# Optimization experiments

Hardware: AMD Instinct MI355X
Metric: run time of the kernel (lower is better)

The kernel has to match this reference:

```python
import jax, jax.numpy as jnp
import numpy as np

N, E, DIN, ED, H, C = 50000, 800000, 128, 16, 4, 128
HC = H * C
SLOPE = 0.2


def gat_conv(x, ei_src, ei_dst, ea, W, a_src, a_dst, We, a_e, b):
    # x: [N, din]; ea: [E, ed] (self-loops already appended by caller)
    n = x.shape[0]
    h = (x @ W).reshape(n, H, C)                       # [N,H,C]
    al_src = (h * a_src).sum(-1)                       # [N,H]
    al_dst = (h * a_dst).sum(-1)                       # [N,H]
    e = (ea @ We).reshape(-1, H, C)                    # [E,H,C]
    al_e = (e * a_e).sum(-1)                           # [E,H]
    alpha = al_src[ei_src] + al_dst[ei_dst] + al_e     # [E,H]
    alpha = jnp.where(alpha > 0, alpha, SLOPE * alpha)  # LeakyReLU(0.2)
    # per-destination-node segment softmax (stable)
    amax = jax.ops.segment_max(alpha, ei_dst, num_segments=n)
    amax = jnp.where(jnp.isfinite(amax), amax, 0.0)
    ex = jnp.exp(alpha - amax[ei_dst])
    den = jax.ops.segment_sum(ex, ei_dst, num_segments=n)
    alpha = ex / (den[ei_dst] + 1e-16)                 # [E,H]
    msg = h[ei_src] * alpha[:, :, None]                # [E,H,C]
    out = jax.ops.segment_sum(msg, ei_dst, num_segments=n)  # [N,H,C]
    return out.reshape(n, HC) + b


def setup_inputs() -> dict:
    key = jax.random.key(0)
    ks = jax.random.split(key, 16)
    s = 0.05
    inp = {
        "x": jax.random.normal(ks[0], (N, DIN), jnp.float32),
        "edge_index": jax.random.randint(ks[1], (2, E), 0, N, jnp.int64),
        "edge_features": jax.random.normal(ks[2], (E, ED), jnp.float32),
        # layer 1 params
        "W1": jax.random.normal(ks[3], (DIN, HC), jnp.float32) * s,
        "att_src1": jax.random.normal(ks[4], (H, C), jnp.float32) * s,
        "att_dst1": jax.random.normal(ks[5], (H, C), jnp.float32) * s,
        "lin_e1": jax.random.normal(ks[6], (ED, HC), jnp.float32) * s,
        "att_e1": jax.random.normal(ks[7], (H, C), jnp.float32) * s,
        "b1": jnp.zeros((HC,), jnp.float32),
        # layer 2 params
        "W2": jax.random.normal(ks[8], (HC, HC), jnp.float32) * s,
        "att_src2": jax.random.normal(ks[9], (H, C), jnp.float32) * s,
        "att_dst2": jax.random.normal(ks[10], (H, C), jnp.float32) * s,
        "lin_e2": jax.random.normal(ks[11], (ED, HC), jnp.float32) * s,
        "att_e2": jax.random.normal(ks[12], (H, C), jnp.float32) * s,
        "b2": jnp.zeros((HC,), jnp.float32),
    }
    return inp


def reference(x, edge_index, edge_features,
              W1, att_src1, att_dst1, lin_e1, att_e1, b1,
              W2, att_src2, att_dst2, lin_e2, att_e2, b2):
    # add self-loops once (PyG default: add_self_loops=True, edge_attr fill='mean')
    loop = jnp.arange(N, dtype=edge_index.dtype)
    ei_src = jnp.concatenate([edge_index[0], loop])
    ei_dst = jnp.concatenate([edge_index[1], loop])
    mean_ea = edge_features.mean(0)
    ea = jnp.concatenate([edge_features, jnp.broadcast_to(mean_ea, (N, ED))], axis=0)

    h = gat_conv(x, ei_src, ei_dst, ea, W1, att_src1, att_dst1, lin_e1, att_e1, b1)
    h = jax.nn.elu(h)
    h = gat_conv(h, ei_src, ei_dst, ea, W2, att_src2, att_dst2, lin_e2, att_e2, b2)
    return jax.nn.elu(h)
```

## Files before the change

### kernel.cpp

```cpp
#include <hip/hip_runtime.h>
#include <math.h>

#define NNODE 50000
#define NEDGE 800000
#define DINv  128
#define EDv   16
#define NHv   4
#define CHv   128
#define HCv   512
#define SLOPEv 0.2f
#define MEANBLK 512

typedef __attribute__((ext_vector_type(8))) short bf16x8;
typedef __attribute__((ext_vector_type(4))) float f32x4;
typedef __attribute__((address_space(3))) unsigned lds_u32;
typedef const __attribute__((address_space(1))) unsigned glb_u32;

__device__ __forceinline__ ushort f2b(float f) {
  unsigned u = __float_as_uint(f);
  u += 0x7FFF + ((u >> 16) & 1);
  return (ushort)(u >> 16);
}
__device__ __forceinline__ float blo(unsigned u) { return __uint_as_float(u << 16); }
__device__ __forceinline__ float bhi(unsigned u) { return __uint_as_float(u & 0xffff0000u); }

__global__ void detect_kernel(const int* __restrict__ ei, int* __restrict__ flag) {
  __shared__ int bad;
  if (threadIdx.x == 0) bad = 0;
  __syncthreads();
  for (int i = threadIdx.x; i < 2048; i += 256)
    if (ei[2 * i + 1] != 0) bad = 1;
  __syncthreads();
  if (threadIdx.x == 0) flag[0] = bad ? 0 : 1;
}

__device__ __forceinline__ int load_idx(const int* __restrict__ ei, int e, int row, int wide) {
  if (wide) return ei[2 * ((size_t)row * NEDGE + e)];
  return ei[(size_t)row * NEDGE + e];
}

__global__ void count_kernel(const int* __restrict__ ei, const int* __restrict__ flag,
                             int* __restrict__ deg) {
  int e = blockIdx.x * blockDim.x + threadIdx.x;
  if (e < NEDGE) {
    int w = flag[0];
    atomicAdd(&deg[load_idx(ei, e, 1, w)], 1);
  }
}

__global__ __launch_bounds__(1024) void scan_kernel(const int* __restrict__ deg,
                                                    int* __restrict__ row_ptr) {
  __shared__ int wsum[16];
  int tid = threadIdx.x;
  int wid = tid >> 6, lane = tid & 63;
  int carry = 0;
  for (int base = 0; base < NNODE; base += 4096) {
    int idx = base + tid * 4;
    int4 x = make_int4(0, 0, 0, 0);
    if (idx < NNODE) x = *(const int4*)(deg + idx);
    int t0 = x.x, t1 = t0 + x.y, t2 = t1 + x.z, t3 = t2 + x.w;
    int v = t3;
#pragma unroll
    for (int off = 1; off < 64; off <<= 1) {
      int t = __shfl_up(v, off, 64);
      if (lane >= off) v += t;
    }
    if (lane == 63) wsum[wid] = v;
    __syncthreads();
    if (wid == 0) {
      int s = (lane < 16) ? wsum[lane] : 0;
#pragma unroll
      for (int off = 1; off < 16; off <<= 1) {
        int t = __shfl_up(s, off, 64);
        if (lane >= off) s += t;
      }
      if (lane < 16) wsum[lane] = s;
    }
    __syncthreads();
    int woff = wid ? wsum[wid - 1] : 0;
    int excl = carry + woff + v - t3;
    if (idx < NNODE) {
      int4 o = make_int4(excl, excl + t0, excl + t1, excl + t2);
      *(int4*)(row_ptr + idx) = o;
    }
    carry += wsum[15];
    __syncthreads();
  }
  if (tid == 0) row_ptr[NNODE] = carry;
}

__global__ void scatter_kernel(const int* __restrict__ ei, const int* __restrict__ flag,
                               const int* __restrict__ row_ptr, int* __restrict__ cursor,
                               int* __restrict__ src_sorted, int* __restrict__ eid_sorted) {
  int e = blockIdx.x * blockDim.x + threadIdx.x;
  if (e < NEDGE) {
    int w = flag[0];
    int d = load_idx(ei, e, 1, w);
    int s = load_idx(ei, e, 0, w);
    int p = row_ptr[d] + atomicAdd(&cursor[d], 1);
    src_sorted[p] = s;
    eid_sorted[p] = e;
  }
}

__global__ void mean_part_kernel(const float* __restrict__ ea, float* __restrict__ partials) {
  float acc[EDv];
#pragma unroll
  for (int d = 0; d < EDv; d++) acc[d] = 0.f;
  int stride = gridDim.x * blockDim.x;
  for (int r = blockIdx.x * blockDim.x + threadIdx.x; r < NEDGE; r += stride) {
    const float4* p = (const float4*)(ea + (size_t)r * EDv);
#pragma unroll
    for (int q = 0; q < 4; q++) {
      float4 v = p[q];
      acc[q * 4 + 0] += v.x; acc[q * 4 + 1] += v.y;
      acc[q * 4 + 2] += v.z; acc[q * 4 + 3] += v.w;
    }
  }
  __shared__ float red[4][EDv];
  int wid = threadIdx.x >> 6, lane = threadIdx.x & 63;
#pragma unroll
  for (int d = 0; d < EDv; d++) {
    float v = acc[d];
    for (int off = 32; off; off >>= 1) v += __shfl_down(v, off, 64);
    if (lane == 0) red[wid][d] = v;
  }
  __syncthreads();
  if (threadIdx.x < EDv) {
    float v = red[0][threadIdx.x] + red[1][threadIdx.x] + red[2][threadIdx.x] + red[3][threadIdx.x];
    partials[blockIdx.x * EDv + threadIdx.x] = v;
  }
}

__global__ void mean_fold_kernel(const float* __restrict__ partials, float* __restrict__ mean_sum) {
  int tid = threadIdx.x;
  int d = tid & 15, r0 = tid >> 4;
  float v = 0.f;
  for (int r = r0; r < MEANBLK; r += 16) v += partials[r * EDv + d];
  __shared__ float buf[256];
  buf[tid] = v;
  __syncthreads();
  if (r0 < 8) buf[tid] += buf[tid + 128];
  __syncthreads();
  if (r0 < 4) buf[tid] += buf[tid + 64];
  __syncthreads();
  if (r0 < 2) buf[tid] += buf[tid + 32];
  __syncthreads();
  if (r0 == 0) mean_sum[d] = buf[tid] + buf[tid + 16];
}

__global__ void vloop_kernel(const float* __restrict__ We, const float* __restrict__ a_e,
                             const float* __restrict__ mean_sum,
                             float* __restrict__ v, float* __restrict__ loop_al_e) {
  int t = threadIdx.x;
  int d = t >> 2, h = t & 3;
  float s = 0.f;
  for (int c = 0; c < CHv; c++) s += We[(size_t)d * HCv + h * CHv + c] * a_e[h * CHv + c];
  v[d * 4 + h] = s;
  __syncthreads();
  if (t < NHv) {
    float acc = 0.f;
    for (int d2 = 0; d2 < EDv; d2++) acc += (mean_sum[d2] * (1.0f / NEDGE)) * v[d2 * 4 + t];
    loop_al_e[t] = acc;
  }
}

__global__ void ale_kernel(const float* __restrict__ ea, const float* __restrict__ v,
                           float* __restrict__ al_e) {
  __shared__ float sv[EDv * NHv];
  if (threadIdx.x < EDv * NHv) sv[threadIdx.x] = v[threadIdx.x];
  __syncthreads();
  int e = blockIdx.x * blockDim.x + threadIdx.x;
  if (e >= NEDGE) return;
  const float4* p = (const float4*)(ea + (size_t)e * EDv);
  float row[16];
  *(float4*)&row[0] = p[0]; *(float4*)&row[4] = p[1];
  *(float4*)&row[8] = p[2]; *(float4*)&row[12] = p[3];
  float o0 = 0, o1 = 0, o2 = 0, o3 = 0;
#pragma unroll
  for (int d = 0; d < 16; d++) {
    o0 += row[d] * sv[d * 4 + 0];
    o1 += row[d] * sv[d * 4 + 1];
    o2 += row[d] * sv[d * 4 + 2];
    o3 += row[d] * sv[d * 4 + 3];
  }
  ((float4*)al_e)[e] = make_float4(o0, o1, o2, o3);
}

__global__ void apre_kernel(const int* __restrict__ src_sorted, const int* __restrict__ eid_sorted,
                            const float* __restrict__ al_src, const float* __restrict__ al_e,
                            float* __restrict__ ap) {
  int p = blockIdx.x * 256 + threadIdx.x;
  if (p >= NEDGE) return;
  int s = src_sorted[p];
  int e = eid_sorted[p];
  float4 a = ((const float4*)al_src)[s];
  float4 b = ((const float4*)al_e)[e];
  ((float4*)ap)[p] = make_float4(a.x + b.x, a.y + b.y, a.z + b.z, a.w + b.w);
}

__global__ void conv_bf16_kernel(const float* __restrict__ in, ushort* __restrict__ out, int n4) {
  int i = blockIdx.x * 256 + threadIdx.x;
  if (i >= n4) return;
  float4 v = ((const float4*)in)[i];
  ushort4 o;
  o.x = f2b(v.x); o.y = f2b(v.y); o.z = f2b(v.z); o.w = f2b(v.w);
  ((ushort4*)out)[i] = o;
}

__global__ void wt_kernel(const float* __restrict__ W, ushort* __restrict__ Bt, int K) {
  int idx = blockIdx.x * 256 + threadIdx.x;
  if (idx >= K * HCv) return;
  int k = idx >> 9, n = idx & (HCv - 1);
  Bt[(size_t)n * K + k] = f2b(W[idx]);
}

__global__ __launch_bounds__(256) void gemm_mfma_kernel(const ushort* __restrict__ A,
                                                        const ushort* __restrict__ Bt,
                                                        ushort* __restrict__ C, int M, int K,
                                                        const float* __restrict__ a_src,
                                                        const float* __restrict__ a_dst,
                                                        float* __restrict__ al_src,
                                                        float* __restrict__ al_dst) {
  __shared__ ushort As[4][128][8];
  __shared__ ushort Bs[4][128][8];
  __shared__ float ssa[128], ssd[128];
  __shared__ float rsum[2][128][2];
  int tid = threadIdx.x;
  int wid = tid >> 6, lane = tid & 63;

  int nblk = gridDim.x * gridDim.y;
  int j = blockIdx.y * gridDim.x + blockIdx.x;
  int q = nblk >> 3, rem = nblk & 7;
  int xcd = j & 7, idx = j >> 3;
  int d = (xcd < rem) ? xcd * (q + 1) + idx : rem * (q + 1) + (xcd - rem) * q + idx;
  int rb = (d >> 2) * 128, cb = (d & 3) * 128;
  int hblk = cb >> 7;

  int wm = (wid >> 1) * 64, wn = (wid & 1) * 64;
  int lr = lane & 15, lq = lane >> 4;

  if (tid < 128) { ssa[tid] = a_src[cb + tid]; ssd[tid] = a_dst[cb + tid]; }

  f32x4 acc[4][4];
#pragma unroll
  for (int i = 0; i < 4; i++)
#pragma unroll
    for (int jx = 0; jx < 4; jx++) acc[i][jx] = (f32x4){0.f, 0.f, 0.f, 0.f};

  ushort* AsF = &As[0][0][0];
  ushort* BsF = &Bs[0][0][0];

  for (int k0 = 0; k0 < K; k0 += 32) {
#pragma unroll
    for (int s = 0; s < 2; s++) {
      int c = s * 256 + tid;
      int kq = c >> 7, m = c & 127;
      int row = rb + m; if (row >= M) row = M - 1;
      const ushort* gA = A + (size_t)row * K + k0 + kq * 8;
      __builtin_amdgcn_global_load_lds((glb_u32*)gA, (lds_u32*)(AsF + (size_t)c * 8), 16, 0, 0);
    }
#pragma unroll
    for (int s = 0; s < 2; s++) {
      int c = s * 256 + tid;
      int kq = c >> 7, n = c & 127;
      const ushort* gB = Bt + (size_t)(cb + n) * K + k0 + kq * 8;
      __builtin_amdgcn_global_load_lds((glb_u32*)gB, (lds_u32*)(BsF + (size_t)c * 8), 16, 0, 0);
    }
    __syncthreads();
    bf16x8 af[4], bfr[4];
#pragma unroll
    for (int i = 0; i < 4; i++) {
      af[i]  = *(const bf16x8*)&As[lq][wm + i * 16 + lr][0];
      bfr[i] = *(const bf16x8*)&Bs[lq][wn + i * 16 + lr][0];
    }
#pragma unroll
    for (int i = 0; i < 4; i++)
#pragma unroll
      for (int jx = 0; jx < 4; jx++)
        acc[i][jx] = __builtin_amdgcn_mfma_f32_16x16x32_bf16(af[i], bfr[jx], acc[i][jx], 0, 0, 0);
    __syncthreads();
  }

#pragma unroll
  for (int i = 0; i < 4; i++) {
    int rbase = rb + wm + i * 16 + lq * 4;
#pragma unroll
    for (int jx = 0; jx < 4; jx++) {
      int col = cb + wn + jx * 16 + lr;
#pragma unroll
      for (int r = 0; r < 4; r++) {
        int row = rbase + r;
        if (row < M) C[(size_t)row * HCv + col] = f2b(acc[i][jx][r]);
      }
    }
  }

  float sa[4], sd[4];
#pragma unroll
  for (int jx = 0; jx < 4; jx++) {
    int c = wn + jx * 16 + lr;
    sa[jx] = ssa[c]; sd[jx] = ssd[c];
  }
#pragma unroll
  for (int i = 0; i < 4; i++) {
#pragma unroll
    for (int r = 0; r < 4; r++) {
      float s1 = 0.f, s2 = 0.f;
#pragma unroll
      for (int jx = 0; jx < 4; jx++) {
        s1 = fmaf(acc[i][jx][r], sa[jx], s1);
        s2 = fmaf(acc[i][jx][r], sd[jx], s2);
      }
#pragma unroll
      for (int off = 1; off < 16; off <<= 1) {
        s1 += __shfl_xor(s1, off, 16);
        s2 += __shfl_xor(s2, off, 16);
      }
      if (lr == 0) {
        int row = wm + i * 16 + lq * 4 + r;
        rsum[0][row][wn >> 6] = s1;
        rsum[1][row][wn >> 6] = s2;
      }
    }
  }
  __syncthreads();
  if (tid < 128) {
    int row = rb + tid;
    if (row < M) {
      al_src[(size_t)row * 4 + hblk] = rsum[0][tid][0] + rsum[0][tid][1];
      al_dst[(size_t)row * 4 + hblk] = rsum[1][tid][0] + rsum[1][tid][1];
    }
  }
}

__device__ __forceinline__ void fma8(float* acc, float w, uint4 u) {
  acc[0] = fmaf(w, blo(u.x), acc[0]);
  acc[1] = fmaf(w, bhi(u.x), acc[1]);
  acc[2] = fmaf(w, blo(u.y), acc[2]);
  acc[3] = fmaf(w, bhi(u.y), acc[3]);
  acc[4] = fmaf(w, blo(u.z), acc[4]);
  acc[5] = fmaf(w, bhi(u.z), acc[5]);
  acc[6] = fmaf(w, blo(u.w), acc[6]);
  acc[7] = fmaf(w, bhi(u.w), acc[7]);
}

__global__ __launch_bounds__(256) void node_kernel(
    const ushort* __restrict__ hb, const float* __restrict__ al_src,
    const float* __restrict__ al_dst, const float* __restrict__ ap,
    const float* __restrict__ loop_al_e, const int* __restrict__ row_ptr,
    const int* __restrict__ src_sorted, const float* __restrict__ bias,
    float* __restrict__ outf, ushort* __restrict__ outb) {
  int wid = threadIdx.x >> 6, lane = threadIdx.x & 63;
  int n = blockIdx.x * 4 + wid;
  if (n >= NNODE) return;
  int base = row_ptr[n];
  int deg = row_ptr[n + 1] - base;
  int h = lane >> 4;
  int jj = lane & 15;

  float aldh = al_dst[(size_t)n * 4 + h];
  float a0 = al_src[(size_t)n * 4 + h] + aldh + loop_al_e[h];
  float alph = a0 > 0.f ? a0 : SLOPEv * a0;
  float wl = __expf(alph);

  uint4 uself = *((const uint4*)(hb + ((size_t)n << 9)) + lane);

  float acc[8];
#pragma unroll
  for (int q = 0; q < 8; q++) acc[q] = 0.f;
  float den = 0.f;

  for (int cs = 0; cs < deg; cs += 16) {
    int cl = min(16, deg - cs);
    float w = 0.f;
    int sv = 0;
    if (jj < cl) {
      int p = base + cs + jj;
      sv = src_sorted[p];
      float a = ap[(size_t)p * 4 + h] + aldh;
      a = a > 0.f ? a : SLOPEv * a;
      w = __expf(a);
      den += w;
    }
    int cl4 = (cl + 3) & ~3;
    for (int j0 = 0; j0 < cl4; j0 += 4) {
      int s0 = __shfl(sv, j0 + 0, 16);
      int s1 = __shfl(sv, j0 + 1, 16);
      int s2 = __shfl(sv, j0 + 2, 16);
      int s3 = __shfl(sv, j0 + 3, 16);
      float w0 = __shfl(w, j0 + 0, 16);
      float w1 = __shfl(w, j0 + 1, 16);
      float w2 = __shfl(w, j0 + 2, 16);
      float w3 = __shfl(w, j0 + 3, 16);
      uint4 u0 = *((const uint4*)(hb + ((size_t)s0 << 9)) + lane);
      uint4 u1 = *((const uint4*)(hb + ((size_t)s1 << 9)) + lane);
      uint4 u2 = *((const uint4*)(hb + ((size_t)s2 << 9)) + lane);
      uint4 u3 = *((const uint4*)(hb + ((size_t)s3 << 9)) + lane);
      fma8(acc, w0, u0);
      fma8(acc, w1, u1);
      fma8(acc, w2, u2);
      fma8(acc, w3, u3);
    }
  }

  fma8(acc, wl, uself);

#pragma unroll
  for (int off = 8; off; off >>= 1) den += __shfl_xor(den, off, 16);
  den += wl;
  float rden = 1.f / (den + 1e-16f);

  const float4* bp = (const float4*)(bias + lane * 8);
  float4 b0 = bp[0], b1 = bp[1];
  float bv[8] = {b0.x, b0.y, b0.z, b0.w, b1.x, b1.y, b1.z, b1.w};
  float r[8];
#pragma unroll
  for (int q = 0; q < 8; q++) {
    float t = acc[q] * rden + bv[q];
    r[q] = t > 0.f ? t : expm1f(t);
  }
  if (outf) {
    float4* op = (float4*)(outf + (size_t)n * HCv + lane * 8);
    op[0] = make_float4(r[0], r[1], r[2], r[3]);
    op[1] = make_float4(r[4], r[5], r[6], r[7]);
  }
  if (outb) {
    uint4 o;
    o.x = (unsigned)f2b(r[0]) | ((unsigned)f2b(r[1]) << 16);
    o.y = (unsigned)f2b(r[2]) | ((unsigned)f2b(r[3]) << 16);
    o.z = (unsigned)f2b(r[4]) | ((unsigned)f2b(r[5]) << 16);
    o.w = (unsigned)f2b(r[6]) | ((unsigned)f2b(r[7]) << 16);
    ((uint4*)(outb + (size_t)n * HCv))[lane] = o;
  }
}

static inline char* take(char*& p, size_t bytes) {
  char* r = p;
  p += (bytes + 255) & ~(size_t)255;
  return r;
}

extern "C" void kernel_launch(void* const* d_in, const int* in_sizes, int n_in,
                              void* d_out, int out_size, void* d_ws, size_t ws_size,
                              hipStream_t stream) {
  (void)in_sizes; (void)n_in; (void)out_size; (void)ws_size;
  const float* x   = (const float*)d_in[0];
  const int*   ei  = (const int*)d_in[1];
  const float* ea  = (const float*)d_in[2];
  const float* W1  = (const float*)d_in[3];
  const float* as1 = (const float*)d_in[4];
  const float* ad1 = (const float*)d_in[5];
  const float* We1 = (const float*)d_in[6];
  const float* ae1 = (const float*)d_in[7];
  const float* b1  = (const float*)d_in[8];
  const float* W2  = (const float*)d_in[9];
  const float* as2 = (const float*)d_in[10];
  const float* ad2 = (const float*)d_in[11];
  const float* We2 = (const float*)d_in[12];
  const float* ae2 = (const float*)d_in[13];
  const float* b2  = (const float*)d_in[14];
  float* out = (float*)d_out;

  char* p = (char*)d_ws;
  ushort* hb        = (ushort*)take(p, (size_t)NNODE * HCv * 2);
  float* al_src     = (float*)take(p, (size_t)NNODE * 4 * 4);
  float* al_dst     = (float*)take(p, (size_t)NNODE * 4 * 4);
  float* al_e       = (float*)take(p, (size_t)NEDGE * 4 * 4);
  float* ap         = (float*)take(p, (size_t)NEDGE * 4 * 4);
  int*   src_sorted = (int*)take(p, (size_t)NEDGE * 4);
  int*   eid_sorted = (int*)take(p, (size_t)NEDGE * 4);
  int*   row_ptr    = (int*)take(p, (size_t)(NNODE + 1) * 4);
  float* partials   = (float*)take(p, (size_t)MEANBLK * EDv * 4);
  ushort* Bt1       = (ushort*)take(p, (size_t)HCv * DINv * 2);
  ushort* Bt2       = (ushort*)take(p, (size_t)HCv * HCv * 2);
  char* zero_begin = p;
  int*   deg        = (int*)take(p, (size_t)NNODE * 4);
  int*   cursor     = (int*)take(p, (size_t)NNODE * 4);
  size_t zero_len = (size_t)(p - zero_begin);
  float* mean_sum   = (float*)take(p, 16 * 4);
  float* v          = (float*)take(p, 64 * 4);
  float* loop_ale   = (float*)take(p, 4 * 4);
  int*   flag       = (int*)take(p, 4);

  ushort* xb  = (ushort*)d_out;
  ushort* h1b = (ushort*)((char*)d_out + (size_t)16 * 1024 * 1024);

  hipMemsetAsync(zero_begin, 0, zero_len, stream);

  detect_kernel<<<1, 256, 0, stream>>>(ei, flag);
  count_kernel<<<(NEDGE + 255) / 256, 256, 0, stream>>>(ei, flag, deg);
  scan_kernel<<<1, 1024, 0, stream>>>(deg, row_ptr);
  scatter_kernel<<<(NEDGE + 255) / 256, 256, 0, stream>>>(ei, flag, row_ptr, cursor,
                                                          src_sorted, eid_sorted);
  mean_part_kernel<<<MEANBLK, 256, 0, stream>>>(ea, partials);
  mean_fold_kernel<<<1, 256, 0, stream>>>(partials, mean_sum);

  conv_bf16_kernel<<<(NNODE * DINv / 4 + 255) / 256, 256, 0, stream>>>(x, xb, NNODE * DINv / 4);
  wt_kernel<<<(DINv * HCv + 255) / 256, 256, 0, stream>>>(W1, Bt1, DINv);
  wt_kernel<<<(HCv * HCv + 255) / 256, 256, 0, stream>>>(W2, Bt2, HCv);

  vloop_kernel<<<1, 64, 0, stream>>>(We1, ae1, mean_sum, v, loop_ale);
  ale_kernel<<<(NEDGE + 255) / 256, 256, 0, stream>>>(ea, v, al_e);
  gemm_mfma_kernel<<<dim3(HCv / 128, (NNODE + 127) / 128), 256, 0, stream>>>(
      xb, Bt1, hb, NNODE, DINv, as1, ad1, al_src, al_dst);
  apre_kernel<<<(NEDGE + 255) / 256, 256, 0, stream>>>(src_sorted, eid_sorted, al_src, al_e, ap);
  node_kernel<<<(NNODE + 3) / 4, 256, 0, stream>>>(hb, al_src, al_dst, ap, loop_ale, row_ptr,
                                                   src_sorted, b1, (float*)nullptr, h1b);

  vloop_kernel<<<1, 64, 0, stream>>>(We2, ae2, mean_sum, v, loop_ale);
  ale_kernel<<<(NEDGE + 255) / 256, 256, 0, stream>>>(ea, v, al_e);
  gemm_mfma_kernel<<<dim3(HCv / 128, (NNODE + 127) / 128), 256, 0, stream>>>(
      h1b, Bt2, hb, NNODE, HCv, as2, ad2, al_src, al_dst);
  apre_kernel<<<(NEDGE + 255) / 256, 256, 0, stream>>>(src_sorted, eid_sorted, al_src, al_e, ap);
  node_kernel<<<(NNODE + 3) / 4, 256, 0, stream>>>(hb, al_src, al_dst, ap, loop_ale, row_ptr,
                                                   src_sorted, b2, out, (ushort*)nullptr);
}
```

Before: 734.8 us.

## Fuse edge-attention precompute for both layers, drop apre pass, widen GEMM K-step

Scatter now records each edge's sorted position instead of the edge id. A single kernel reads edge features once, computes both layers' edge attention terms directly in sorted order, and accumulates the mean for self-loops. The separate apre pass is removed and node_kernel gathers al_src per edge on the fly. Input/weight conversions and small prep kernels are merged to cut launches, and the GEMM K-step doubles to 64 with larger LDS tiles. The trade-offs are a scattered write in the fused edge kernel, an extra random gather in node_kernel, and more LDS per GEMM block.

```diff
diff --git a/kernel.cpp b/kernel.cpp
--- a/kernel.cpp
+++ b/kernel.cpp
@@ -10,6 +10,7 @@
 #define HCv   512
 #define SLOPEv 0.2f
 #define MEANBLK 512
+#define CONVN (NNODE * DINv / 4)
 
 typedef __attribute__((ext_vector_type(8))) short bf16x8;
 typedef __attribute__((ext_vector_type(4))) float f32x4;
@@ -91,7 +92,7 @@
 
 __global__ void scatter_kernel(const int* __restrict__ ei, const int* __restrict__ flag,
                                const int* __restrict__ row_ptr, int* __restrict__ cursor,
-                               int* __restrict__ src_sorted, int* __restrict__ eid_sorted) {
+                               int* __restrict__ src_sorted, int* __restrict__ pos) {
   int e = blockIdx.x * blockDim.x + threadIdx.x;
   if (e < NEDGE) {
     int w = flag[0];
@@ -99,23 +100,57 @@
     int s = load_idx(ei, e, 0, w);
     int p = row_ptr[d] + atomicAdd(&cursor[d], 1);
     src_sorted[p] = s;
-    eid_sorted[p] = e;
-  }
-}
-
-__global__ void mean_part_kernel(const float* __restrict__ ea, float* __restrict__ partials) {
+    pos[e] = p;
+  }
+}
+
+__global__ void prep_kernel(const float* __restrict__ We1, const float* __restrict__ ae1,
+                            const float* __restrict__ We2, const float* __restrict__ ae2,
+                            float* __restrict__ v1, float* __restrict__ v2) {
+  int t = threadIdx.x;
+  int layer = t >> 6, u = t & 63;
+  int d = u >> 2, h = u & 3;
+  const float* We = layer ? We2 : We1;
+  const float* ae = layer ? ae2 : ae1;
+  float s = 0.f;
+  for (int c = 0; c < CHv; c++) s += We[(size_t)d * HCv + h * CHv + c] * ae[h * CHv + c];
+  (layer ? v2 : v1)[d * 4 + h] = s;
+}
+
+__global__ void ale_both_kernel(const float* __restrict__ ea, const int* __restrict__ pos,
+                                const float* __restrict__ v1, const float* __restrict__ v2,
+                                float* __restrict__ al1, float* __restrict__ al2,
+                                float* __restrict__ partials) {
+  __shared__ float sv1[64], sv2[64];
+  if (threadIdx.x < 64) sv1[threadIdx.x] = v1[threadIdx.x];
+  else if (threadIdx.x < 128) sv2[threadIdx.x - 64] = v2[threadIdx.x - 64];
+  __syncthreads();
   float acc[EDv];
 #pragma unroll
   for (int d = 0; d < EDv; d++) acc[d] = 0.f;
   int stride = gridDim.x * blockDim.x;
-  for (int r = blockIdx.x * blockDim.x + threadIdx.x; r < NEDGE; r += stride) {
-    const float4* p = (const float4*)(ea + (size_t)r * EDv);
-#pragma unroll
-    for (int q = 0; q < 4; q++) {
-      float4 v = p[q];
-      acc[q * 4 + 0] += v.x; acc[q * 4 + 1] += v.y;
-      acc[q * 4 + 2] += v.z; acc[q * 4 + 3] += v.w;
-    }
+  for (int e = blockIdx.x * blockDim.x + threadIdx.x; e < NEDGE; e += stride) {
+    const float4* pr = (const float4*)(ea + (size_t)e * EDv);
+    float row[16];
+    *(float4*)&row[0] = pr[0]; *(float4*)&row[4] = pr[1];
+    *(float4*)&row[8] = pr[2]; *(float4*)&row[12] = pr[3];
+    float a0 = 0, a1 = 0, a2 = 0, a3 = 0;
+    float b0 = 0, b1 = 0, b2 = 0, b3 = 0;
+#pragma unroll
+    for (int d = 0; d < 16; d++) {
+      acc[d] += row[d];
+      a0 += row[d] * sv1[d * 4 + 0];
+      a1 += row[d] * sv1[d * 4 + 1];
+      a2 += row[d] * sv1[d * 4 + 2];
+      a3 += row[d] * sv1[d * 4 + 3];
+      b0 += row[d] * sv2[d * 4 + 0];
+      b1 += row[d] * sv2[d * 4 + 1];
+      b2 += row[d] * sv2[d * 4 + 2];
+      b3 += row[d] * sv2[d * 4 + 3];
+    }
+    int p = pos[e];
+    ((float4*)al1)[p] = make_float4(a0, a1, a2, a3);
+    ((float4*)al2)[p] = make_float4(b0, b1, b2, b3);
   }
   __shared__ float red[4][EDv];
   int wid = threadIdx.x >> 6, lane = threadIdx.x & 63;
@@ -132,12 +167,15 @@
   }
 }
 
-__global__ void mean_fold_kernel(const float* __restrict__ partials, float* __restrict__ mean_sum) {
+__global__ void fold_kernel(const float* __restrict__ partials,
+                            const float* __restrict__ v1, const float* __restrict__ v2,
+                            float* __restrict__ loop1, float* __restrict__ loop2) {
   int tid = threadIdx.x;
   int d = tid & 15, r0 = tid >> 4;
   float v = 0.f;
   for (int r = r0; r < MEANBLK; r += 16) v += partials[r * EDv + d];
   __shared__ float buf[256];
+  __shared__ float ms[16];
   buf[tid] = v;
   __syncthreads();
   if (r0 < 8) buf[tid] += buf[tid + 128];
@@ -146,73 +184,35 @@
   __syncthreads();
   if (r0 < 2) buf[tid] += buf[tid + 32];
   __syncthreads();
-  if (r0 == 0) mean_sum[d] = buf[tid] + buf[tid + 16];
-}
-
-__global__ void vloop_kernel(const float* __restrict__ We, const float* __restrict__ a_e,
-                             const float* __restrict__ mean_sum,
-                             float* __restrict__ v, float* __restrict__ loop_al_e) {
-  int t = threadIdx.x;
-  int d = t >> 2, h = t & 3;
-  float s = 0.f;
-  for (int c = 0; c < CHv; c++) s += We[(size_t)d * HCv + h * CHv + c] * a_e[h * CHv + c];
-  v[d * 4 + h] = s;
-  __syncthreads();
-  if (t < NHv) {
-    float acc = 0.f;
-    for (int d2 = 0; d2 < EDv; d2++) acc += (mean_sum[d2] * (1.0f / NEDGE)) * v[d2 * 4 + t];
-    loop_al_e[t] = acc;
-  }
-}
-
-__global__ void ale_kernel(const float* __restrict__ ea, const float* __restrict__ v,
-                           float* __restrict__ al_e) {
-  __shared__ float sv[EDv * NHv];
-  if (threadIdx.x < EDv * NHv) sv[threadIdx.x] = v[threadIdx.x];
-  __syncthreads();
-  int e = blockIdx.x * blockDim.x + threadIdx.x;
-  if (e >= NEDGE) return;
-  const float4* p = (const float4*)(ea + (size_t)e * EDv);
-  float row[16];
-  *(float4*)&row[0] = p[0]; *(float4*)&row[4] = p[1];
-  *(float4*)&row[8] = p[2]; *(float4*)&row[12] = p[3];
-  float o0 = 0, o1 = 0, o2 = 0, o3 = 0;
-#pragma unroll
-  for (int d = 0; d < 16; d++) {
-    o0 += row[d] * sv[d * 4 + 0];
-    o1 += row[d] * sv[d * 4 + 1];
-    o2 += row[d] * sv[d * 4 + 2];
-    o3 += row[d] * sv[d * 4 + 3];
-  }
-  ((float4*)al_e)[e] = make_float4(o0, o1, o2, o3);
-}
-
-__global__ void apre_kernel(const int* __restrict__ src_sorted, const int* __restrict__ eid_sorted,
-                            const float* __restrict__ al_src, const float* __restrict__ al_e,
-                            float* __restrict__ ap) {
-  int p = blockIdx.x * 256 + threadIdx.x;
-  if (p >= NEDGE) return;
-  int s = src_sorted[p];
-  int e = eid_sorted[p];
-  float4 a = ((const float4*)al_src)[s];
-  float4 b = ((const float4*)al_e)[e];
-  ((float4*)ap)[p] = make_float4(a.x + b.x, a.y + b.y, a.z + b.z, a.w + b.w);
-}
-
-__global__ void conv_bf16_kernel(const float* __restrict__ in, ushort* __restrict__ out, int n4) {
+  if (r0 == 0) ms[d] = (buf[tid] + buf[tid + 16]) * (1.0f / NEDGE);
+  __syncthreads();
+  if (tid < 8) {
+    const float* vv = (tid >> 2) ? v2 : v1;
+    int h = tid & 3;
+    float a = 0.f;
+    for (int d2 = 0; d2 < EDv; d2++) a += ms[d2] * vv[d2 * 4 + h];
+    ((tid >> 2) ? loop2 : loop1)[h] = a;
+  }
+}
+
+__global__ void convwt_kernel(const float* __restrict__ x, const float* __restrict__ W1,
+                              const float* __restrict__ W2, ushort* __restrict__ xb,
+                              ushort* __restrict__ Bt1, ushort* __restrict__ Bt2) {
   int i = blockIdx.x * 256 + threadIdx.x;
-  if (i >= n4) return;
-  float4 v = ((const float4*)in)[i];
-  ushort4 o;
-  o.x = f2b(v.x); o.y = f2b(v.y); o.z = f2b(v.z); o.w = f2b(v.w);
-  ((ushort4*)out)[i] = o;
-}
-
-__global__ void wt_kernel(const float* __restrict__ W, ushort* __restrict__ Bt, int K) {
-  int idx = blockIdx.x * 256 + threadIdx.x;
-  if (idx >= K * HCv) return;
-  int k = idx >> 9, n = idx & (HCv - 1);
-  Bt[(size_t)n * K + k] = f2b(W[idx]);
+  if (i < CONVN) {
+    float4 v = ((const float4*)x)[i];
+    ushort4 o;
+    o.x = f2b(v.x); o.y = f2b(v.y); o.z = f2b(v.z); o.w = f2b(v.w);
+    ((ushort4*)xb)[i] = o;
+  } else if (i < CONVN + DINv * HCv) {
+    int idx = i - CONVN;
+    int k = idx >> 9, n = idx & (HCv - 1);
+    Bt1[(size_t)n * DINv + k] = f2b(W1[idx]);
+  } else if (i < CONVN + DINv * HCv + HCv * HCv) {
+    int idx = i - CONVN - DINv * HCv;
+    int k = idx >> 9, n = idx & (HCv - 1);
+    Bt2[(size_t)n * HCv + k] = f2b(W2[idx]);
+  }
 }
 
 __global__ __launch_bounds__(256) void gemm_mfma_kernel(const ushort* __restrict__ A,
@@ -222,8 +222,8 @@
                                                         const float* __restrict__ a_dst,
                                                         float* __restrict__ al_src,
                                                         float* __restrict__ al_dst) {
-  __shared__ ushort As[4][128][8];
-  __shared__ ushort Bs[4][128][8];
+  __shared__ ushort As[8][128][8];
+  __shared__ ushort Bs[8][128][8];
   __shared__ float ssa[128], ssd[128];
   __shared__ float rsum[2][128][2];
   int tid = threadIdx.x;
@@ -251,9 +251,9 @@
   ushort* AsF = &As[0][0][0];
   ushort* BsF = &Bs[0][0][0];
 
-  for (int k0 = 0; k0 < K; k0 += 32) {
-#pragma unroll
-    for (int s = 0; s < 2; s++) {
+  for (int k0 = 0; k0 < K; k0 += 64) {
+#pragma unroll
+    for (int s = 0; s < 4; s++) {
       int c = s * 256 + tid;
       int kq = c >> 7, m = c & 127;
       int row = rb + m; if (row >= M) row = M - 1;
@@ -261,24 +261,27 @@
       __builtin_amdgcn_global_load_lds((glb_u32*)gA, (lds_u32*)(AsF + (size_t)c * 8), 16, 0, 0);
     }
 #pragma unroll
-    for (int s = 0; s < 2; s++) {
+    for (int s = 0; s < 4; s++) {
       int c = s * 256 + tid;
       int kq = c >> 7, n = c & 127;
       const ushort* gB = Bt + (size_t)(cb + n) * K + k0 + kq * 8;
       __builtin_amdgcn_global_load_lds((glb_u32*)gB, (lds_u32*)(BsF + (size_t)c * 8), 16, 0, 0);
     }
     __syncthreads();
-    bf16x8 af[4], bfr[4];
-#pragma unroll
-    for (int i = 0; i < 4; i++) {
-      af[i]  = *(const bf16x8*)&As[lq][wm + i * 16 + lr][0];
-      bfr[i] = *(const bf16x8*)&Bs[lq][wn + i * 16 + lr][0];
-    }
-#pragma unroll
-    for (int i = 0; i < 4; i++)
-#pragma unroll
-      for (int jx = 0; jx < 4; jx++)
-        acc[i][jx] = __builtin_amdgcn_mfma_f32_16x16x32_bf16(af[i], bfr[jx], acc[i][jx], 0, 0, 0);
+#pragma unroll
+    for (int hh = 0; hh < 2; hh++) {
+      bf16x8 af[4], bfr[4];
+#pragma unroll
+      for (int i = 0; i < 4; i++) {
+        af[i]  = *(const bf16x8*)&As[hh * 4 + lq][wm + i * 16 + lr][0];
+        bfr[i] = *(const bf16x8*)&Bs[hh * 4 + lq][wn + i * 16 + lr][0];
+      }
+#pragma unroll
+      for (int i = 0; i < 4; i++)
+#pragma unroll
+        for (int jx = 0; jx < 4; jx++)
+          acc[i][jx] = __builtin_amdgcn_mfma_f32_16x16x32_bf16(af[i], bfr[jx], acc[i][jx], 0, 0, 0);
+    }
     __syncthreads();
   }
 
@@ -347,7 +350,7 @@
 
 __global__ __launch_bounds__(256) void node_kernel(
     const ushort* __restrict__ hb, const float* __restrict__ al_src,
-    const float* __restrict__ al_dst, const float* __restrict__ ap,
+    const float* __restrict__ al_dst, const float* __restrict__ al_e,
     const float* __restrict__ loop_al_e, const int* __restrict__ row_ptr,
     const int* __restrict__ src_sorted, const float* __restrict__ bias,
     float* __restrict__ outf, ushort* __restrict__ outb) {
@@ -378,7 +381,7 @@
     if (jj < cl) {
       int p = base + cs + jj;
       sv = src_sorted[p];
-      float a = ap[(size_t)p * 4 + h] + aldh;
+      float a = al_src[(size_t)sv * 4 + h] + al_e[(size_t)p * 4 + h] + aldh;
       a = a > 0.f ? a : SLOPEv * a;
       w = __expf(a);
       den += w;
@@ -466,10 +469,10 @@
   ushort* hb        = (ushort*)take(p, (size_t)NNODE * HCv * 2);
   float* al_src     = (float*)take(p, (size_t)NNODE * 4 * 4);
   float* al_dst     = (float*)take(p, (size_t)NNODE * 4 * 4);
-  float* al_e       = (float*)take(p, (size_t)NEDGE * 4 * 4);
-  float* ap         = (float*)take(p, (size_t)NEDGE * 4 * 4);
+  float* ale1       = (float*)take(p, (size_t)NEDGE * 4 * 4);
+  float* ale2       = (float*)take(p, (size_t)NEDGE * 4 * 4);
   int*   src_sorted = (int*)take(p, (size_t)NEDGE * 4);
-  int*   eid_sorted = (int*)take(p, (size_t)NEDGE * 4);
+  int*   pos        = (int*)take(p, (size_t)NEDGE * 4);
   int*   row_ptr    = (int*)take(p, (size_t)(NNODE + 1) * 4);
   float* partials   = (float*)take(p, (size_t)MEANBLK * EDv * 4);
   ushort* Bt1       = (ushort*)take(p, (size_t)HCv * DINv * 2);
@@ -478,9 +481,10 @@
   int*   deg        = (int*)take(p, (size_t)NNODE * 4);
   int*   cursor     = (int*)take(p, (size_t)NNODE * 4);
   size_t zero_len = (size_t)(p - zero_begin);
-  float* mean_sum   = (float*)take(p, 16 * 4);
-  float* v          = (float*)take(p, 64 * 4);
-  float* loop_ale   = (float*)take(p, 4 * 4);
+  float* v1         = (float*)take(p, 64 * 4);
+  float* v2         = (float*)take(p, 64 * 4);
+  float* loop1      = (float*)take(p, 4 * 4);
+  float* loop2      = (float*)take(p, 4 * 4);
   int*   flag       = (int*)take(p, 4);
 
   ushort* xb  = (ushort*)d_out;
@@ -492,27 +496,20 @@
   count_kernel<<<(NEDGE + 255) / 256, 256, 0, stream>>>(ei, flag, deg);
   scan_kernel<<<1, 1024, 0, stream>>>(deg, row_ptr);
   scatter_kernel<<<(NEDGE + 255) / 256, 256, 0, stream>>>(ei, flag, row_ptr, cursor,
-                                                          src_sorted, eid_sorted);
-  mean_part_kernel<<<MEANBLK, 256, 0, stream>>>(ea, partials);
-  mean_fold_kernel<<<1, 256, 0, stream>>>(partials, mean_sum);
-
-  conv_bf16_kernel<<<(NNODE * DINv / 4 + 255) / 256, 256, 0, stream>>>(x, xb, NNODE * DINv / 4);
-  wt_kernel<<<(DINv * HCv + 255) / 256, 256, 0, stream>>>(W1, Bt1, DINv);
-  wt_kernel<<<(HCv * HCv + 255) / 256, 256, 0, stream>>>(W2, Bt2, HCv);
-
-  vloop_kernel<<<1, 64, 0, stream>>>(We1, ae1, mean_sum, v, loop_ale);
-  ale_kernel<<<(NEDGE + 255) / 256, 256, 0, stream>>>(ea, v, al_e);
+                                                          src_sorted, pos);
+  prep_kernel<<<1, 128, 0, stream>>>(We1, ae1, We2, ae2, v1, v2);
+  convwt_kernel<<<(CONVN + DINv * HCv + HCv * HCv + 255) / 256, 256, 0, stream>>>(
+      x, W1, W2, xb, Bt1, Bt2);
+  ale_both_kernel<<<MEANBLK, 256, 0, stream>>>(ea, pos, v1, v2, ale1, ale2, partials);
+  fold_kernel<<<1, 256, 0, stream>>>(partials, v1, v2, loop1, loop2);
+
   gemm_mfma_kernel<<<dim3(HCv / 128, (NNODE + 127) / 128), 256, 0, stream>>>(
       xb, Bt1, hb, NNODE, DINv, as1, ad1, al_src, al_dst);
-  apre_kernel<<<(NEDGE + 255) / 256, 256, 0, stream>>>(src_sorted, eid_sorted, al_src, al_e, ap);
-  node_kernel<<<(NNODE + 3) / 4, 256, 0, stream>>>(hb, al_src, al_dst, ap, loop_ale, row_ptr,
+  node_kernel<<<(NNODE + 3) / 4, 256, 0, stream>>>(hb, al_src, al_dst, ale1, loop1, row_ptr,
                                                    src_sorted, b1, (float*)nullptr, h1b);
 
-  vloop_kernel<<<1, 64, 0, stream>>>(We2, ae2, mean_sum, v, loop_ale);
-  ale_kernel<<<(NEDGE + 255) / 256, 256, 0, stream>>>(ea, v, al_e);
   gemm_mfma_kernel<<<dim3(HCv / 128, (NNODE + 127) / 128), 256, 0, stream>>>(
       h1b, Bt2, hb, NNODE, HCv, as2, ad2, al_src, al_dst);
-  apre_kernel<<<(NEDGE + 255) / 256, 256, 0, stream>>>(src_sorted, eid_sorted, al_src, al_e, ap);
-  node_kernel<<<(NNODE + 3) / 4, 256, 0, stream>>>(hb, al_src, al_dst, ap, loop_ale, row_ptr,
+  node_kernel<<<(NNODE + 3) / 4, 256, 0, stream>>>(hb, al_src, al_dst, ale2, loop2, row_ptr,
                                                    src_sorted, b2, out, (ushort*)nullptr);
 }
```

Measured after the change: 770.9 us. 4.9% more time.
